# Kernel tuning notes

Hardware: AMD Instinct MI355X
Metric: run time of the kernel (lower is better)

Reference implementation:

```python
import jax, jax.numpy as jnp
import numpy as np

N_LAYERS = 200
KSIZE = 7
L_IN = 1388
FC_IN = 188   # 1388 - 200*6
FC_OUT = 91


def setup_inputs() -> dict:
    key = jax.random.key(0)
    k_x, k_w, k_b, k_fw, k_fb = jax.random.split(key, 5)
    B = 1024
    x = jax.random.normal(k_x, (B, L_IN), dtype=jnp.float32)
    # Conv1d(1,1,7) weights: torch default init U(-s, s) with s = 1/sqrt(in_ch*k) = 1/sqrt(7)
    s = 1.0 / np.sqrt(KSIZE)
    conv_w = jax.random.uniform(k_w, (N_LAYERS, KSIZE), dtype=jnp.float32, minval=-s, maxval=s)
    conv_b = jax.random.uniform(k_b, (N_LAYERS,), dtype=jnp.float32, minval=-s, maxval=s)
    sf = 1.0 / np.sqrt(FC_IN)
    fc_w = jax.random.uniform(k_fw, (FC_OUT, FC_IN), dtype=jnp.float32, minval=-sf, maxval=sf)
    fc_b = jax.random.uniform(k_fb, (FC_OUT,), dtype=jnp.float32, minval=-sf, maxval=sf)
    return {"x": x, "conv_w": conv_w, "conv_b": conv_b, "fc_w": fc_w, "fc_b": fc_b}


def _conv1(h, w, b):
    # h: [B, L]; cross-correlation with taps w[0..6], valid padding -> [B, L-6]
    L_out = h.shape[1] - (KSIZE - 1)
    acc = w[0] * h[:, 0:L_out]
    for k in range(1, KSIZE):
        acc = acc + w[k] * h[:, k:k + L_out]
    return acc + b


def reference(x, conv_w, conv_b, fc_w, fc_b):
    h = x  # unsqueeze(1) is implicit: single channel handled as [B, L]
    for i in range(N_LAYERS):
        h = _conv1(h, conv_w[i], conv_b[i])
        if i < N_LAYERS - 1:  # last ReLU was popped in the torch module
            h = jax.nn.relu(h)
    # Linear(188, 91) applied to the length dim, then Sigmoid; squeeze channel dim
    out = jax.nn.sigmoid(h @ fc_w.T + fc_b)  # [B, 91]
    return out
```

## Files before the change

kernel.cpp:

```cpp
#include <hip/hip_runtime.h>
#include <math.h>

#define N_LAYERS 200
#define KSIZE 7
#define L_IN 1388
#define FC_IN 188
#define FC_OUT 91
#define NT 256
#define NSTAGES 13

typedef float v2f __attribute__((ext_vector_type(2)));

constexpr int s_lo(int s)  { return 16 * s; }
constexpr int s_hi(int s)  { return (s < 12) ? 16 * s + 16 : N_LAYERS; }
constexpr int lin_(int s)  { return L_IN - 6 * s_lo(s); }
constexpr int lout_(int s) { return L_IN - 6 * s_hi(s); }
constexpr int cut_(int s)  { return lout_(s) / 2; }
constexpr int marg_(int s) { return 6 * (s_hi(s) - s_lo(s)); }
constexpr int s_R(int s) {
    const int a = cut_(s) + marg_(s);
    const int b = lin_(s) - cut_(s);
    const int m = (a > b) ? a : b;
    return (m + 63) / 64;
}
constexpr int s_Re(int s) { return (s_R(s) + 1) & ~1; }

__device__ __forceinline__ float dpp_next(float v) {
    return __int_as_float(
        __builtin_amdgcn_mov_dpp(__float_as_int(v), 0x130, 0xf, 0xf, true));
}
__device__ __forceinline__ v2f dpp_next2(v2f v) {
    v2f o; o.x = dpp_next(v.x); o.y = dpp_next(v.y); return o;
}

__device__ __forceinline__ v2f pk_fma(v2f a, v2f b, v2f c) {
    return __builtin_elementwise_fma(a, b, c);
}
__device__ __forceinline__ v2f pk_max0(v2f a) {
    return __builtin_elementwise_max(a, (v2f)(0.0f));
}

struct WG { v2f w2[28]; v2f b2[4]; };

__device__ __forceinline__ void load_wg(WG& wg, const v2f* wbuf2,
                                        const v2f* bbuf2, int g) {
#pragma unroll
    for (int t = 0; t < 28; ++t) wg.w2[t] = wbuf2[g * 28 + t];
#pragma unroll
    for (int j = 0; j < 4; ++j) wg.b2[j] = bbuf2[g * 4 + j];
}

template<int R, bool NR3>
__device__ __forceinline__ void run4(v2f (&r2)[6], const WG& wg) {
    constexpr int P = R / 2;
#pragma unroll
    for (int jj = 0; jj < 4; ++jj) {
        v2f h[3];
        {
            constexpr int L1 = (P < 3) ? P : 3;
            v2f l1[L1];
#pragma unroll
            for (int t = 0; t < L1; ++t) l1[t] = dpp_next2(r2[t]);
#pragma unroll
            for (int t = 0; t < L1; ++t) h[t] = l1[t];
            if constexpr (P == 2) h[2] = dpp_next2(l1[0]);
        }
        v2f M[P + 2];
#pragma unroll
        for (int j = 0; j < P + 2; ++j) {
            const v2f a = (j < P) ? r2[j] : h[j - P];
            const v2f b = (j + 1 < P) ? r2[j + 1] : h[j + 1 - P];
            v2f m; m.x = a.y; m.y = b.x;
            M[j] = m;
        }
        const bool relu = !(NR3 && jj == 3);
#pragma unroll
        for (int j = 0; j < P; ++j) {
            v2f acc = wg.b2[jj];
#pragma unroll
            for (int d = 0; d < KSIZE; ++d) {
                v2f src;
                if (d % 2 == 0) {
                    const int m = j + d / 2;
                    src = (m < P) ? r2[m] : h[m - P];
                } else {
                    src = M[j + (d - 1) / 2];
                }
                acc = pk_fma(wg.w2[jj * 7 + d], src, acc);
            }
            r2[j] = relu ? pk_max0(acc) : acc;
        }
    }
}

template<int R, bool FINAL>
__device__ __forceinline__ void run_stage_g(v2f (&r2)[6], WG& A,
        const v2f* wbuf2, const v2f* bbuf2, int g0, int g1) {
#pragma unroll 1
    for (int g = g0; g < g1; g += 2) {
        WG B;
        load_wg(B, wbuf2, bbuf2, (g + 1 < 50) ? g + 1 : 49);
        run4<R, false>(r2, A);
        load_wg(A, wbuf2, bbuf2, (g + 2 < 50) ? g + 2 : 49);
        run4<R, FINAL>(r2, B);
    }
}

template<int Ro, int Rn>
__device__ __forceinline__ void repack(v2f (&r2)[6], v2f* lbuf2,
                                       int lane, int rwid,
                                       int cut_o, int lout_o, int cut_n)
{
    const int base2  = (rwid ? cut_o : 0) / 2;
    const int bound2 = (rwid ? lout_o : cut_o) / 2;
#pragma unroll
    for (int j = 0; j < Ro / 2; ++j) {
        const int pg = base2 + lane * (Ro / 2) + j;
        if (pg < bound2) lbuf2[pg] = r2[j];
    }
    __syncthreads();
    const int nb2 = (rwid ? cut_n : 0) / 2;
#pragma unroll
    for (int j = 0; j < Rn / 2; ++j) r2[j] = lbuf2[nb2 + lane * (Rn / 2) + j];
    __syncthreads();
}

template<int S>
struct Chain {
    __device__ static __forceinline__ void run(v2f (&r2)[6], WG& A,
        const v2f* wbuf2, const v2f* bbuf2, v2f* lbuf2, int lane, int rwid)
    {
        run_stage_g<s_Re(S), false>(r2, A, wbuf2, bbuf2, 4 * S, 4 * S + 4);
        repack<s_Re(S), s_Re(S + 1)>(r2, lbuf2, lane, rwid,
                                     cut_(S), lout_(S), cut_(S + 1));
        Chain<S + 1>::run(r2, A, wbuf2, bbuf2, lbuf2, lane, rwid);
    }
};

template<>
struct Chain<NSTAGES - 1> {
    __device__ static __forceinline__ void run(v2f (&r2)[6], WG& A,
        const v2f* wbuf2, const v2f* bbuf2, v2f* lbuf2, int lane, int rwid)
    {
        constexpr int R = s_Re(NSTAGES - 1);
        run_stage_g<R, true>(r2, A, wbuf2, bbuf2, 48, 50);
        const int base2  = rwid ? 47 : 0;
        const int bound2 = rwid ? 94 : 47;
#pragma unroll
        for (int j = 0; j < R / 2; ++j) {
            const int pg = base2 + lane * (R / 2) + j;
            if (pg < bound2) lbuf2[pg] = r2[j];
        }
        __syncthreads();
    }
};

__global__ __launch_bounds__(NT, 2) void conv_chain_kernel(
    const float* __restrict__ x,
    const float* __restrict__ conv_w,
    const float* __restrict__ conv_b,
    const float* __restrict__ fc_w,
    const float* __restrict__ fc_b,
    float* __restrict__ out)
{
    __shared__ __align__(16) v2f lbuf2[2][688];
    __shared__ __align__(16) v2f wbuf2[N_LAYERS * KSIZE];
    __shared__ __align__(16) v2f bbuf2[N_LAYERS];

    const int tid   = threadIdx.x;
    const int lane  = tid & 63;
    const int wid   = tid >> 6;
    const int rsel  = wid >> 1;
    const int rwid  = wid & 1;
    const int row   = blockIdx.x * 2 + rsel;

    v2f* lbufr = lbuf2[rsel];

    for (int i = tid; i < N_LAYERS * KSIZE; i += NT) {
        const float v = conv_w[i];
        v2f p; p.x = v; p.y = v; wbuf2[i] = p;
    }
    for (int i = tid; i < N_LAYERS; i += NT) {
        const float v = conv_b[i];
        v2f p; p.x = v; p.y = v; bbuf2[i] = p;
    }

    v2f r2[6];
    const float* xr = x + (size_t)row * L_IN;
    const int c0 = rwid ? cut_(0) : 0;
#pragma unroll
    for (int j = 0; j < 6; ++j) {
        const int p = c0 + lane * 12 + 2 * j;
        v2f v;
        if (p + 1 < L_IN)      v = *(const v2f*)(xr + p);
        else if (p < L_IN)     { v.x = xr[p]; v.y = 0.0f; }
        else                   { v.x = 0.0f;  v.y = 0.0f; }
        r2[j] = v;
    }
    __syncthreads();

    WG A;
    load_wg(A, wbuf2, bbuf2, 0);

    Chain<0>::run(r2, A, wbuf2, bbuf2, lbufr, lane, rwid);

    const int pt = tid & 127;
    if (pt < FC_OUT) {
        float acc = fc_b[pt];
        const float4* wp = (const float4*)(fc_w + pt * FC_IN);
        const float4* hp = (const float4*)lbufr;
#pragma unroll 4
        for (int q = 0; q < FC_IN / 4; ++q) {
            const float4 hv = hp[q];
            const float4 wv = wp[q];
            acc = fmaf(wv.x, hv.x, acc);
            acc = fmaf(wv.y, hv.y, acc);
            acc = fmaf(wv.z, hv.z, acc);
            acc = fmaf(wv.w, hv.w, acc);
        }
        out[(size_t)row * FC_OUT + pt] = 1.0f / (1.0f + expf(-acc));
    }
}

extern "C" void kernel_launch(void* const* d_in, const int* in_sizes, int n_in,
                              void* d_out, int out_size, void* d_ws, size_t ws_size,
                              hipStream_t stream) {
    const float* x      = (const float*)d_in[0];
    const float* conv_w = (const float*)d_in[1];
    const float* conv_b = (const float*)d_in[2];
    const float* fc_w   = (const float*)d_in[3];
    const float* fc_b   = (const float*)d_in[4];
    float* outp = (float*)d_out;

    const int batch = in_sizes[0] / L_IN;
    conv_chain_kernel<<<batch / 2, NT, 0, stream>>>(x, conv_w, conv_b, fc_w, fc_b, outp);
}
```

Before: 113.6 us.

## Process two batch rows per wave to share weight registers and halve block size

New measurement: 148.4 us. 1.31x slower.

```diff
diff --git a/kernel.cpp b/kernel.cpp
--- a/kernel.cpp
+++ b/kernel.cpp
@@ -6,7 +6,7 @@
 #define L_IN 1388
 #define FC_IN 188
 #define FC_OUT 91
-#define NT 256
+#define NT 128
 #define NSTAGES 13
 
 typedef float v2f __attribute__((ext_vector_type(2)));
@@ -51,63 +51,82 @@
 }
 
 template<int R, bool NR3>
-__device__ __forceinline__ void run4(v2f (&r2)[6], const WG& wg) {
+__device__ __forceinline__ void run4(v2f (&ra)[6], v2f (&rb)[6], const WG& wg) {
     constexpr int P = R / 2;
 #pragma unroll
     for (int jj = 0; jj < 4; ++jj) {
-        v2f h[3];
+        v2f ha[3], hb[3];
         {
             constexpr int L1 = (P < 3) ? P : 3;
-            v2f l1[L1];
-#pragma unroll
-            for (int t = 0; t < L1; ++t) l1[t] = dpp_next2(r2[t]);
-#pragma unroll
-            for (int t = 0; t < L1; ++t) h[t] = l1[t];
-            if constexpr (P == 2) h[2] = dpp_next2(l1[0]);
-        }
-        v2f M[P + 2];
+            v2f la[L1], lb[L1];
+#pragma unroll
+            for (int t = 0; t < L1; ++t) {
+                la[t] = dpp_next2(ra[t]);
+                lb[t] = dpp_next2(rb[t]);
+            }
+#pragma unroll
+            for (int t = 0; t < L1; ++t) { ha[t] = la[t]; hb[t] = lb[t]; }
+            if constexpr (P == 2) {
+                ha[2] = dpp_next2(la[0]);
+                hb[2] = dpp_next2(lb[0]);
+            }
+        }
+        v2f Ma[P + 2], Mb[P + 2];
 #pragma unroll
         for (int j = 0; j < P + 2; ++j) {
-            const v2f a = (j < P) ? r2[j] : h[j - P];
-            const v2f b = (j + 1 < P) ? r2[j + 1] : h[j + 1 - P];
-            v2f m; m.x = a.y; m.y = b.x;
-            M[j] = m;
+            {
+                const v2f a = (j < P) ? ra[j] : ha[j - P];
+                const v2f b = (j + 1 < P) ? ra[j + 1] : ha[j + 1 - P];
+                v2f m; m.x = a.y; m.y = b.x; Ma[j] = m;
+            }
+            {
+                const v2f a = (j < P) ? rb[j] : hb[j - P];
+                const v2f b = (j + 1 < P) ? rb[j + 1] : hb[j + 1 - P];
+                v2f m; m.x = a.y; m.y = b.x; Mb[j] = m;
+            }
         }
         const bool relu = !(NR3 && jj == 3);
 #pragma unroll
         for (int j = 0; j < P; ++j) {
-            v2f acc = wg.b2[jj];
+            v2f acca = wg.b2[jj];
+            v2f accb = wg.b2[jj];
 #pragma unroll
             for (int d = 0; d < KSIZE; ++d) {
-                v2f src;
+                v2f sa, sb;
                 if (d % 2 == 0) {
                     const int m = j + d / 2;
-                    src = (m < P) ? r2[m] : h[m - P];
+                    sa = (m < P) ? ra[m] : ha[m - P];
+                    sb = (m < P) ? rb[m] : hb[m - P];
                 } else {
-                    src = M[j + (d - 1) / 2];
+                    sa = Ma[j + (d - 1) / 2];
+                    sb = Mb[j + (d - 1) / 2];
                 }
-                acc = pk_fma(wg.w2[jj * 7 + d], src, acc);
-            }
-            r2[j] = relu ? pk_max0(acc) : acc;
+                const v2f w = wg.w2[jj * 7 + d];
+                acca = pk_fma(w, sa, acca);
+                accb = pk_fma(w, sb, accb);
+            }
+            ra[j] = relu ? pk_max0(acca) : acca;
+            rb[j] = relu ? pk_max0(accb) : accb;
         }
     }
 }
 
 template<int R, bool FINAL>
-__device__ __forceinline__ void run_stage_g(v2f (&r2)[6], WG& A,
+__device__ __forceinline__ void run_stage_g(v2f (&ra)[6], v2f (&rb)[6], WG& A,
         const v2f* wbuf2, const v2f* bbuf2, int g0, int g1) {
 #pragma unroll 1
     for (int g = g0; g < g1; g += 2) {
         WG B;
         load_wg(B, wbuf2, bbuf2, (g + 1 < 50) ? g + 1 : 49);
-        run4<R, false>(r2, A);
+        run4<R, false>(ra, rb, A);
         load_wg(A, wbuf2, bbuf2, (g + 2 < 50) ? g + 2 : 49);
-        run4<R, FINAL>(r2, B);
+        run4<R, FINAL>(ra, rb, B);
     }
 }
 
 template<int Ro, int Rn>
-__device__ __forceinline__ void repack(v2f (&r2)[6], v2f* lbuf2,
+__device__ __forceinline__ void repack(v2f (&ra)[6], v2f (&rb)[6],
+                                       v2f* la, v2f* lb,
                                        int lane, int rwid,
                                        int cut_o, int lout_o, int cut_n)
 {
@@ -116,46 +135,49 @@
 #pragma unroll
     for (int j = 0; j < Ro / 2; ++j) {
         const int pg = base2 + lane * (Ro / 2) + j;
-        if (pg < bound2) lbuf2[pg] = r2[j];
+        if (pg < bound2) { la[pg] = ra[j]; lb[pg] = rb[j]; }
     }
     __syncthreads();
     const int nb2 = (rwid ? cut_n : 0) / 2;
 #pragma unroll
-    for (int j = 0; j < Rn / 2; ++j) r2[j] = lbuf2[nb2 + lane * (Rn / 2) + j];
+    for (int j = 0; j < Rn / 2; ++j) {
+        ra[j] = la[nb2 + lane * (Rn / 2) + j];
+        rb[j] = lb[nb2 + lane * (Rn / 2) + j];
+    }
     __syncthreads();
 }
 
 template<int S>
 struct Chain {
-    __device__ static __forceinline__ void run(v2f (&r2)[6], WG& A,
-        const v2f* wbuf2, const v2f* bbuf2, v2f* lbuf2, int lane, int rwid)
+    __device__ static __forceinline__ void run(v2f (&ra)[6], v2f (&rb)[6], WG& A,
+        const v2f* wbuf2, const v2f* bbuf2, v2f* la, v2f* lb, int lane, int rwid)
     {
-        run_stage_g<s_Re(S), false>(r2, A, wbuf2, bbuf2, 4 * S, 4 * S + 4);
-        repack<s_Re(S), s_Re(S + 1)>(r2, lbuf2, lane, rwid,
+        run_stage_g<s_Re(S), false>(ra, rb, A, wbuf2, bbuf2, 4 * S, 4 * S + 4);
+        repack<s_Re(S), s_Re(S + 1)>(ra, rb, la, lb, lane, rwid,
                                      cut_(S), lout_(S), cut_(S + 1));
-        Chain<S + 1>::run(r2, A, wbuf2, bbuf2, lbuf2, lane, rwid);
+        Chain<S + 1>::run(ra, rb, A, wbuf2, bbuf2, la, lb, lane, rwid);
     }
 };
 
 template<>
 struct Chain<NSTAGES - 1> {
-    __device__ static __forceinline__ void run(v2f (&r2)[6], WG& A,
-        const v2f* wbuf2, const v2f* bbuf2, v2f* lbuf2, int lane, int rwid)
+    __device__ static __forceinline__ void run(v2f (&ra)[6], v2f (&rb)[6], WG& A,
+        const v2f* wbuf2, const v2f* bbuf2, v2f* la, v2f* lb, int lane, int rwid)
     {
         constexpr int R = s_Re(NSTAGES - 1);
-        run_stage_g<R, true>(r2, A, wbuf2, bbuf2, 48, 50);
+        run_stage_g<R, true>(ra, rb, A, wbuf2, bbuf2, 48, 50);
         const int base2  = rwid ? 47 : 0;
         const int bound2 = rwid ? 94 : 47;
 #pragma unroll
         for (int j = 0; j < R / 2; ++j) {
             const int pg = base2 + lane * (R / 2) + j;
-            if (pg < bound2) lbuf2[pg] = r2[j];
+            if (pg < bound2) { la[pg] = ra[j]; lb[pg] = rb[j]; }
         }
         __syncthreads();
     }
 };
 
-__global__ __launch_bounds__(NT, 2) void conv_chain_kernel(
+__global__ __launch_bounds__(NT, 1) void conv_chain_kernel(
     const float* __restrict__ x,
     const float* __restrict__ conv_w,
     const float* __restrict__ conv_b,
@@ -169,12 +191,9 @@
 
     const int tid   = threadIdx.x;
     const int lane  = tid & 63;
-    const int wid   = tid >> 6;
-    const int rsel  = wid >> 1;
-    const int rwid  = wid & 1;
-    const int row   = blockIdx.x * 2 + rsel;
-
-    v2f* lbufr = lbuf2[rsel];
+    const int rwid  = tid >> 6;
+    const int rowa  = blockIdx.x * 2;
+    const int rowb  = rowa + 1;
 
     for (int i = tid; i < N_LAYERS * KSIZE; i += NT) {
         const float v = conv_w[i];
@@ -185,40 +204,55 @@
         v2f p; p.x = v; p.y = v; bbuf2[i] = p;
     }
 
-    v2f r2[6];
-    const float* xr = x + (size_t)row * L_IN;
+    v2f ra[6], rb[6];
+    const float* xa = x + (size_t)rowa * L_IN;
+    const float* xb = x + (size_t)rowb * L_IN;
     const int c0 = rwid ? cut_(0) : 0;
 #pragma unroll
     for (int j = 0; j < 6; ++j) {
         const int p = c0 + lane * 12 + 2 * j;
-        v2f v;
-        if (p + 1 < L_IN)      v = *(const v2f*)(xr + p);
-        else if (p < L_IN)     { v.x = xr[p]; v.y = 0.0f; }
-        else                   { v.x = 0.0f;  v.y = 0.0f; }
-        r2[j] = v;
+        v2f va, vb;
+        if (p + 1 < L_IN) {
+            va = *(const v2f*)(xa + p);
+            vb = *(const v2f*)(xb + p);
+        } else if (p < L_IN) {
+            va.x = xa[p]; va.y = 0.0f;
+            vb.x = xb[p]; vb.y = 0.0f;
+        } else {
+            va.x = 0.0f; va.y = 0.0f;
+            vb = va;
+        }
+        ra[j] = va; rb[j] = vb;
     }
     __syncthreads();
 
     WG A;
     load_wg(A, wbuf2, bbuf2, 0);
 
-    Chain<0>::run(r2, A, wbuf2, bbuf2, lbufr, lane, rwid);
-
-    const int pt = tid & 127;
-    if (pt < FC_OUT) {
-        float acc = fc_b[pt];
-        const float4* wp = (const float4*)(fc_w + pt * FC_IN);
-        const float4* hp = (const float4*)lbufr;
+    Chain<0>::run(ra, rb, A, wbuf2, bbuf2, lbuf2[0], lbuf2[1], lane, rwid);
+
+    if (tid < FC_OUT) {
+        const float4* wp = (const float4*)(fc_w + tid * FC_IN);
+        const float4* ha = (const float4*)lbuf2[0];
+        const float4* hb = (const float4*)lbuf2[1];
+        float acca = fc_b[tid];
+        float accb = acca;
 #pragma unroll 4
         for (int q = 0; q < FC_IN / 4; ++q) {
-            const float4 hv = hp[q];
             const float4 wv = wp[q];
-            acc = fmaf(wv.x, hv.x, acc);
-            acc = fmaf(wv.y, hv.y, acc);
-            acc = fmaf(wv.z, hv.z, acc);
-            acc = fmaf(wv.w, hv.w, acc);
-        }
-        out[(size_t)row * FC_OUT + pt] = 1.0f / (1.0f + expf(-acc));
+            const float4 va = ha[q];
+            const float4 vb = hb[q];
+            acca = fmaf(wv.x, va.x, acca);
+            accb = fmaf(wv.x, vb.x, accb);
+            acca = fmaf(wv.y, va.y, acca);
+            accb = fmaf(wv.y, vb.y, accb);
+            acca = fmaf(wv.z, va.z, acca);
+            accb = fmaf(wv.z, vb.z, accb);
+            acca = fmaf(wv.w, va.w, acca);
+            accb = fmaf(wv.w, vb.w, accb);
+        }
+        out[(size_t)rowa * FC_OUT + tid] = 1.0f / (1.0f + expf(-acca));
+        out[(size_t)rowb * FC_OUT + tid] = 1.0f / (1.0f + expf(-accb));
     }
 }
 
```

## Split each lane's chunk into two halves packed in v2f lanes

Applied to the files above, without the earlier changes.

Result: no change. 114.0 us (+0.4%).

```diff
diff --git a/kernel.cpp b/kernel.cpp
--- a/kernel.cpp
+++ b/kernel.cpp
@@ -8,6 +8,7 @@
 #define FC_OUT 91
 #define NT 256
 #define NSTAGES 13
+#define LBUF_N 1376
 
 typedef float v2f __attribute__((ext_vector_type(2)));
 
@@ -55,23 +56,16 @@
     constexpr int P = R / 2;
 #pragma unroll
     for (int jj = 0; jj < 4; ++jj) {
-        v2f h[3];
+        v2f C[6];
         {
-            constexpr int L1 = (P < 3) ? P : 3;
-            v2f l1[L1];
-#pragma unroll
-            for (int t = 0; t < L1; ++t) l1[t] = dpp_next2(r2[t]);
-#pragma unroll
-            for (int t = 0; t < L1; ++t) h[t] = l1[t];
-            if constexpr (P == 2) h[2] = dpp_next2(l1[0]);
-        }
-        v2f M[P + 2];
-#pragma unroll
-        for (int j = 0; j < P + 2; ++j) {
-            const v2f a = (j < P) ? r2[j] : h[j - P];
-            const v2f b = (j + 1 < P) ? r2[j + 1] : h[j + 1 - P];
-            v2f m; m.x = a.y; m.y = b.x;
-            M[j] = m;
+            constexpr int NC = (P < 6) ? P : 6;
+#pragma unroll
+            for (int t = 0; t < NC; ++t) {
+                v2f c; c.x = r2[t].y; c.y = dpp_next(r2[t].x);
+                C[t] = c;
+            }
+#pragma unroll
+            for (int t = NC; t < 6; ++t) C[t] = dpp_next2(C[t - P]);
         }
         const bool relu = !(NR3 && jj == 3);
 #pragma unroll
@@ -79,13 +73,8 @@
             v2f acc = wg.b2[jj];
 #pragma unroll
             for (int d = 0; d < KSIZE; ++d) {
-                v2f src;
-                if (d % 2 == 0) {
-                    const int m = j + d / 2;
-                    src = (m < P) ? r2[m] : h[m - P];
-                } else {
-                    src = M[j + (d - 1) / 2];
-                }
+                const int m = j + d;
+                const v2f src = (m < P) ? r2[m] : C[m - P];
                 acc = pk_fma(wg.w2[jj * 7 + d], src, acc);
             }
             r2[j] = relu ? pk_max0(acc) : acc;
@@ -107,49 +96,56 @@
 }
 
 template<int Ro, int Rn>
-__device__ __forceinline__ void repack(v2f (&r2)[6], v2f* lbuf2,
+__device__ __forceinline__ void repack(v2f (&r2)[6], float* lb,
                                        int lane, int rwid,
                                        int cut_o, int lout_o, int cut_n)
 {
-    const int base2  = (rwid ? cut_o : 0) / 2;
-    const int bound2 = (rwid ? lout_o : cut_o) / 2;
-#pragma unroll
-    for (int j = 0; j < Ro / 2; ++j) {
-        const int pg = base2 + lane * (Ro / 2) + j;
-        if (pg < bound2) lbuf2[pg] = r2[j];
+    constexpr int Po = Ro / 2, Pn = Rn / 2;
+    const int base  = rwid ? cut_o : 0;
+    const int bound = rwid ? lout_o : cut_o;
+    const int o = base + lane * Ro;
+#pragma unroll
+    for (int j = 0; j < Po; ++j) {
+        if (o + j < bound)      lb[o + j]      = r2[j].x;
+        if (o + j + Po < bound) lb[o + j + Po] = r2[j].y;
     }
     __syncthreads();
-    const int nb2 = (rwid ? cut_n : 0) / 2;
-#pragma unroll
-    for (int j = 0; j < Rn / 2; ++j) r2[j] = lbuf2[nb2 + lane * (Rn / 2) + j];
+    const int nb = (rwid ? cut_n : 0) + lane * Rn;
+#pragma unroll
+    for (int j = 0; j < Pn; ++j) {
+        v2f v; v.x = lb[nb + j]; v.y = lb[nb + j + Pn];
+        r2[j] = v;
+    }
     __syncthreads();
 }
 
 template<int S>
 struct Chain {
     __device__ static __forceinline__ void run(v2f (&r2)[6], WG& A,
-        const v2f* wbuf2, const v2f* bbuf2, v2f* lbuf2, int lane, int rwid)
+        const v2f* wbuf2, const v2f* bbuf2, float* lbufr, int lane, int rwid)
     {
         run_stage_g<s_Re(S), false>(r2, A, wbuf2, bbuf2, 4 * S, 4 * S + 4);
-        repack<s_Re(S), s_Re(S + 1)>(r2, lbuf2, lane, rwid,
+        repack<s_Re(S), s_Re(S + 1)>(r2, lbufr, lane, rwid,
                                      cut_(S), lout_(S), cut_(S + 1));
-        Chain<S + 1>::run(r2, A, wbuf2, bbuf2, lbuf2, lane, rwid);
+        Chain<S + 1>::run(r2, A, wbuf2, bbuf2, lbufr, lane, rwid);
     }
 };
 
 template<>
 struct Chain<NSTAGES - 1> {
     __device__ static __forceinline__ void run(v2f (&r2)[6], WG& A,
-        const v2f* wbuf2, const v2f* bbuf2, v2f* lbuf2, int lane, int rwid)
+        const v2f* wbuf2, const v2f* bbuf2, float* lbufr, int lane, int rwid)
     {
         constexpr int R = s_Re(NSTAGES - 1);
+        constexpr int P = R / 2;
         run_stage_g<R, true>(r2, A, wbuf2, bbuf2, 48, 50);
-        const int base2  = rwid ? 47 : 0;
-        const int bound2 = rwid ? 94 : 47;
-#pragma unroll
-        for (int j = 0; j < R / 2; ++j) {
-            const int pg = base2 + lane * (R / 2) + j;
-            if (pg < bound2) lbuf2[pg] = r2[j];
+        const int base  = rwid ? 94 : 0;
+        const int bound = rwid ? 188 : 94;
+        const int o = base + lane * R;
+#pragma unroll
+        for (int j = 0; j < P; ++j) {
+            if (o + j < bound)     lbufr[o + j]     = r2[j].x;
+            if (o + j + P < bound) lbufr[o + j + P] = r2[j].y;
         }
         __syncthreads();
     }
@@ -163,7 +159,7 @@
     const float* __restrict__ fc_b,
     float* __restrict__ out)
 {
-    __shared__ __align__(16) v2f lbuf2[2][688];
+    __shared__ __align__(16) float lbuf[2][LBUF_N];
     __shared__ __align__(16) v2f wbuf2[N_LAYERS * KSIZE];
     __shared__ __align__(16) v2f bbuf2[N_LAYERS];
 
@@ -174,7 +170,7 @@
     const int rwid  = wid & 1;
     const int row   = blockIdx.x * 2 + rsel;
 
-    v2f* lbufr = lbuf2[rsel];
+    float* lbufr = lbuf[rsel];
 
     for (int i = tid; i < N_LAYERS * KSIZE; i += NT) {
         const float v = conv_w[i];
@@ -184,17 +180,19 @@
         const float v = conv_b[i];
         v2f p; p.x = v; p.y = v; bbuf2[i] = p;
     }
+    for (int i = tid; i < 2 * LBUF_N; i += NT) lbuf[0][i] = 0.0f;
 
     v2f r2[6];
     const float* xr = x + (size_t)row * L_IN;
+    constexpr int R0 = s_Re(0), P0 = R0 / 2;
     const int c0 = rwid ? cut_(0) : 0;
-#pragma unroll
-    for (int j = 0; j < 6; ++j) {
-        const int p = c0 + lane * 12 + 2 * j;
+    const int o0 = c0 + lane * R0;
+#pragma unroll
+    for (int j = 0; j < P0; ++j) {
+        const int pa = o0 + j, pb = o0 + j + P0;
         v2f v;
-        if (p + 1 < L_IN)      v = *(const v2f*)(xr + p);
-        else if (p < L_IN)     { v.x = xr[p]; v.y = 0.0f; }
-        else                   { v.x = 0.0f;  v.y = 0.0f; }
+        v.x = (pa < L_IN) ? xr[pa] : 0.0f;
+        v.y = (pb < L_IN) ? xr[pb] : 0.0f;
         r2[j] = v;
     }
     __syncthreads();
```
